# Kernel tuning notes

Measured on AMD Instinct MI355X. Metric: run time of the kernel, lower is better.

Reference implementation:

```python
import jax, jax.numpy as jnp
import numpy as np

# ---- static tree structure (matches the 4-ary adjacency passed at init) ----
N = 145  # total nodes incl. root 0; output has N-1 = 144 channels
PARENT = np.array([(i - 1) // 4 for i in range(1, N)], dtype=np.int64)  # parent node id of node i (i=1..N-1)
DEPTH = np.zeros(N, dtype=np.int64)
for i in range(1, N):
    DEPTH[i] = DEPTH[(i - 1) // 4] + 1
MAX_DEPTH = int(DEPTH.max())
PARENT_J = jnp.asarray(PARENT)          # [N-1] segment id (= parent node) per non-root node
DEPTH_J = jnp.asarray(DEPTH[1:])        # [N-1] depth of each non-root node (>=1)


def tree_softmax(x):
    """x: [B, N-1, H, W] logits. Sibling-group softmax along channel axis,
    then multiply each node's prob by the product of its ancestors' probs."""
    xt = jnp.moveaxis(x, 1, 0)  # [N-1, B, H, W]: node axis leading for segment ops
    seg = PARENT_J
    # segmented (per-sibling-group) numerically stable softmax
    m = jax.ops.segment_max(xt, seg, num_segments=N)[seg]
    e = jnp.exp(xt - m)
    s = jax.ops.segment_sum(e, seg, num_segments=N)[seg]
    p = e / s  # [N-1, B, H, W]
    # level-by-level multiplicative propagation: res[i] = p[i] * res[parent(i)]
    res = p  # depth-1 nodes (root children) are already final
    for d in range(2, MAX_DEPTH + 1):
        # pad with ones at node 0 (root) so we can gather by node id
        resp = jnp.concatenate([jnp.ones_like(res[:1]), res], axis=0)  # [N, B, H, W]
        gathered = resp[PARENT_J]  # each node's parent's (already-final) result
        mask = (DEPTH_J == d).reshape(-1, 1, 1, 1)
        res = jnp.where(mask, res * gathered, res)
    return jnp.moveaxis(res, 0, 1)  # [B, N-1, H, W]


def setup_inputs() -> dict:
    key = jax.random.key(0)
    x = jax.random.normal(key, (4, 144, 256, 256), dtype=jnp.float32)
    return {"x": x}


def reference(x):
    return tree_softmax(x)
```

## Files before the change

### kernel.cpp

```cpp
#include <hip/hip_runtime.h>


struct f2 { float v[2]; };

__device__ __forceinline__ void grp4(const f2 in[4], const f2 pr, f2 out[4]) {
#pragma unroll
    for (int k = 0; k < 2; ++k) {
        float a = in[0].v[k], b = in[1].v[k], c = in[2].v[k], d = in[3].v[k];
        float m = fmaxf(fmaxf(a, b), fmaxf(c, d));
        float e0 = __expf(a - m);
        float e1 = __expf(b - m);
        float e2 = __expf(c - m);
        float e3 = __expf(d - m);
        float s = e0 + e1 + e2 + e3;
        float f = pr.v[k] / s;
        out[0].v[k] = e0 * f;
        out[1].v[k] = e1 * f;
        out[2].v[k] = e2 * f;
        out[3].v[k] = e3 * f;
    }
}

__global__ __launch_bounds__(256) void tree_softmax_kernel(
        const float* __restrict__ x, float* __restrict__ y) {
    const int HW = 256 * 256;
    const int C  = 144;
    const int cs = HW / 2;

    int tid = blockIdx.x * 256 + threadIdx.x;
    int b   = tid >> 15;
    int rem = tid & 32767;
    size_t base = (size_t)b * C * HW + (size_t)rem * 2;

    const f2* __restrict__ xp = reinterpret_cast<const f2*>(x + base);
    f2*       __restrict__ yp = reinterpret_cast<f2*>(y + base);

    f2 in[4], o[4];

    f2 r1[4];
    f2 one; one.v[0] = 1.0f; one.v[1] = 1.0f;
#pragma unroll
    for (int c = 0; c < 4; ++c) in[c] = xp[c * cs];
    grp4(in, one, r1);
#pragma unroll
    for (int c = 0; c < 4; ++c) yp[c * cs] = r1[c];

    f2 r2[16];
#pragma unroll
    for (int p = 0; p < 4; ++p) {
#pragma unroll
        for (int c = 0; c < 4; ++c) in[c] = xp[(4 + 4 * p + c) * cs];
        grp4(in, r1[p], o);
#pragma unroll
        for (int c = 0; c < 4; ++c) {
            yp[(4 + 4 * p + c) * cs] = o[c];
            r2[4 * p + c] = o[c];
        }
    }

    f2 keep[15];
#pragma unroll
    for (int p = 0; p < 16; ++p) {
#pragma unroll
        for (int c = 0; c < 4; ++c) in[c] = xp[(20 + 4 * p + c) * cs];
        grp4(in, r2[p], o);
#pragma unroll
        for (int c = 0; c < 4; ++c) {
            int idx = 4 * p + c;
            yp[(20 + idx) * cs] = o[c];
            if (idx < 15) keep[idx] = o[c];
        }
    }

#pragma unroll
    for (int p = 0; p < 15; ++p) {
#pragma unroll
        for (int c = 0; c < 4; ++c) in[c] = xp[(84 + 4 * p + c) * cs];
        grp4(in, keep[p], o);
#pragma unroll
        for (int c = 0; c < 4; ++c) yp[(84 + 4 * p + c) * cs] = o[c];
    }
}

extern "C" void kernel_launch(void* const* d_in, const int* in_sizes, int n_in,
                              void* d_out, int out_size, void* d_ws, size_t ws_size,
                              hipStream_t stream) {
    const float* x = (const float*)d_in[0];
    float* y = (float*)d_out;
    const int threads = 256;
    const int blocks  = (4 * 256 * 256 / 2) / threads;
    tree_softmax_kernel<<<blocks, threads, 0, stream>>>(x, y);
}
```

Before: 252.5 us.

## Process one pixel per thread and use nontemporal stores for outputs

```diff
diff --git a/kernel.cpp b/kernel.cpp
--- a/kernel.cpp
+++ b/kernel.cpp
@@ -1,73 +1,64 @@
 #include <hip/hip_runtime.h>
 
 
-struct f2 { float v[2]; };
-
-__device__ __forceinline__ void grp4(const f2 in[4], const f2 pr, f2 out[4]) {
-#pragma unroll
-    for (int k = 0; k < 2; ++k) {
-        float a = in[0].v[k], b = in[1].v[k], c = in[2].v[k], d = in[3].v[k];
-        float m = fmaxf(fmaxf(a, b), fmaxf(c, d));
-        float e0 = __expf(a - m);
-        float e1 = __expf(b - m);
-        float e2 = __expf(c - m);
-        float e3 = __expf(d - m);
-        float s = e0 + e1 + e2 + e3;
-        float f = pr.v[k] / s;
-        out[0].v[k] = e0 * f;
-        out[1].v[k] = e1 * f;
-        out[2].v[k] = e2 * f;
-        out[3].v[k] = e3 * f;
-    }
+__device__ __forceinline__ void grp4s(const float in[4], float pr, float out[4]) {
+    float m = fmaxf(fmaxf(in[0], in[1]), fmaxf(in[2], in[3]));
+    float e0 = __expf(in[0] - m);
+    float e1 = __expf(in[1] - m);
+    float e2 = __expf(in[2] - m);
+    float e3 = __expf(in[3] - m);
+    float f = pr / (e0 + e1 + e2 + e3);
+    out[0] = e0 * f;
+    out[1] = e1 * f;
+    out[2] = e2 * f;
+    out[3] = e3 * f;
 }
 
 __global__ __launch_bounds__(256) void tree_softmax_kernel(
         const float* __restrict__ x, float* __restrict__ y) {
     const int HW = 256 * 256;
     const int C  = 144;
-    const int cs = HW / 2;
 
     int tid = blockIdx.x * 256 + threadIdx.x;
-    int b   = tid >> 15;
-    int rem = tid & 32767;
-    size_t base = (size_t)b * C * HW + (size_t)rem * 2;
+    int b   = tid >> 16;
+    int rem = tid & 65535;
+    size_t base = (size_t)b * C * HW + (size_t)rem;
 
-    const f2* __restrict__ xp = reinterpret_cast<const f2*>(x + base);
-    f2*       __restrict__ yp = reinterpret_cast<f2*>(y + base);
+    const float* __restrict__ xp = x + base;
+    float*       __restrict__ yp = y + base;
 
-    f2 in[4], o[4];
+    float in[4], o[4];
 
-    f2 r1[4];
-    f2 one; one.v[0] = 1.0f; one.v[1] = 1.0f;
+    float r1[4];
 #pragma unroll
-    for (int c = 0; c < 4; ++c) in[c] = xp[c * cs];
-    grp4(in, one, r1);
+    for (int c = 0; c < 4; ++c) in[c] = xp[c * HW];
+    grp4s(in, 1.0f, r1);
 #pragma unroll
-    for (int c = 0; c < 4; ++c) yp[c * cs] = r1[c];
+    for (int c = 0; c < 4; ++c) __builtin_nontemporal_store(r1[c], &yp[c * HW]);
 
-    f2 r2[16];
+    float r2[16];
 #pragma unroll
     for (int p = 0; p < 4; ++p) {
 #pragma unroll
-        for (int c = 0; c < 4; ++c) in[c] = xp[(4 + 4 * p + c) * cs];
-        grp4(in, r1[p], o);
+        for (int c = 0; c < 4; ++c) in[c] = xp[(4 + 4 * p + c) * HW];
+        grp4s(in, r1[p], o);
 #pragma unroll
         for (int c = 0; c < 4; ++c) {
-            yp[(4 + 4 * p + c) * cs] = o[c];
+            __builtin_nontemporal_store(o[c], &yp[(4 + 4 * p + c) * HW]);
             r2[4 * p + c] = o[c];
         }
     }
 
-    f2 keep[15];
+    float keep[15];
 #pragma unroll
     for (int p = 0; p < 16; ++p) {
 #pragma unroll
-        for (int c = 0; c < 4; ++c) in[c] = xp[(20 + 4 * p + c) * cs];
-        grp4(in, r2[p], o);
+        for (int c = 0; c < 4; ++c) in[c] = xp[(20 + 4 * p + c) * HW];
+        grp4s(in, r2[p], o);
 #pragma unroll
         for (int c = 0; c < 4; ++c) {
             int idx = 4 * p + c;
-            yp[(20 + idx) * cs] = o[c];
+            __builtin_nontemporal_store(o[c], &yp[(20 + idx) * HW]);
             if (idx < 15) keep[idx] = o[c];
         }
     }
@@ -75,10 +66,11 @@
 #pragma unroll
     for (int p = 0; p < 15; ++p) {
 #pragma unroll
-        for (int c = 0; c < 4; ++c) in[c] = xp[(84 + 4 * p + c) * cs];
-        grp4(in, keep[p], o);
+        for (int c = 0; c < 4; ++c) in[c] = xp[(84 + 4 * p + c) * HW];
+        grp4s(in, keep[p], o);
 #pragma unroll
-        for (int c = 0; c < 4; ++c) yp[(84 + 4 * p + c) * cs] = o[c];
+        for (int c = 0; c < 4; ++c)
+            __builtin_nontemporal_store(o[c], &yp[(84 + 4 * p + c) * HW]);
     }
 }
 
@@ -88,6 +80,6 @@
     const float* x = (const float*)d_in[0];
     float* y = (float*)d_out;
     const int threads = 256;
-    const int blocks  = (4 * 256 * 256 / 2) / threads;
+    const int blocks  = (4 * 256 * 256) / threads;
     tree_softmax_kernel<<<blocks, threads, 0, stream>>>(x, y);
 }
```

After: 261.1 us. 3.4% more time.
